# Kernel tuning notes

Hardware: AMD Instinct MI355X
Metric: run time of the kernel (lower is better)

Reference implementation:

```python
import jax, jax.numpy as jnp
import numpy as np


def setup_inputs() -> dict:
    key = jax.random.key(0)
    k1, k2, k3 = jax.random.split(key, 3)
    B, S, D = 2, 2048, 1024
    N_COMPRESS, RANK = 64, 64
    x = jax.random.normal(k1, (B, S, D), dtype=jnp.float32)
    router_w = jax.random.normal(k2, (N_COMPRESS, D), dtype=jnp.float32) * (1.0 / np.sqrt(D))
    # compress neurons (orthogonal-init in torch; gaussian scaled is fine for a numeric baseline)
    neurons = jax.random.normal(k3, (N_COMPRESS, D, RANK), dtype=jnp.float32) * (1.0 / np.sqrt(D))
    return {"x": x, "router_w": router_w, "neurons": neurons}


TOP_K = 2


def reference(x, router_w, neurons):
    # x: [B,S,D], router_w: [N,D], neurons: [N,D,R]
    B, S, D = x.shape
    R = neurons.shape[-1]
    scores = jnp.einsum('bsd,nd->bsn', x, router_w)            # [B,S,N]
    topk_scores, topk_idx = jax.lax.top_k(scores, TOP_K)       # [B,S,K]
    topk_weights = jax.nn.softmax(topk_scores, axis=-1)        # [B,S,K]
    output = jnp.zeros((B, S, R), dtype=x.dtype)
    for i in range(TOP_K):  # small fixed loop, mirrors original slot-wise combine
        idx = topk_idx[:, :, i]                                # [B,S]
        sel = neurons[idx]                                     # [B,S,D,R] gather
        proj = jnp.einsum('bsd,bsdr->bsr', x, sel)             # per-token matvec
        output = output + topk_weights[:, :, i:i + 1] * proj
    return output, topk_idx, topk_weights
```

## Files before the change

### kernel.cpp

```cpp
#include <hip/hip_runtime.h>
#include <hip/hip_bf16.h>


typedef unsigned short u16;
typedef unsigned int u32;
typedef __attribute__((ext_vector_type(8))) short short8;
typedef __attribute__((ext_vector_type(4))) float f32x4;

__device__ __forceinline__ float bf2f(u16 u) {
    u32 v = ((u32)u) << 16; float f; __builtin_memcpy(&f, &v, 4); return f;
}
__device__ __forceinline__ u16 f2bf(float f) {
    u32 u; __builtin_memcpy(&u, &f, 4);
    u32 r = u + 0x7fff + ((u >> 16) & 1);
    return (u16)(r >> 16);
}
__device__ __forceinline__ u32 pack2(float a, float b) {
    return ((u32)f2bf(b) << 16) | (u32)f2bf(a);
}

#define T_TOKENS 4096
#define DDIM 1024
#define NEXP 64
#define RDIM 64
#define LCAP 1024
#define OUT_IDX_OFF 262144
#define OUT_W_OFF 270336

struct LdBF {
    const u16* p;
    __device__ __forceinline__ float4 ld4(size_t i) const {
        ushort4 v = *(const ushort4*)(p + i);
        return make_float4(bf2f(v.x), bf2f(v.y), bf2f(v.z), bf2f(v.w));
    }
    __device__ __forceinline__ float ld1(size_t i) const { return bf2f(p[i]); }
};
struct LdF32 {
    const float* p;
    __device__ __forceinline__ float4 ld4(size_t i) const { return *(const float4*)(p + i); }
    __device__ __forceinline__ float ld1(size_t i) const { return p[i]; }
};

__device__ __forceinline__ int detect_f32(const u16* x, int* lds_cnt) {
    if (threadIdx.x == 0) *lds_cnt = 0;
    __syncthreads();
    if (threadIdx.x < 256) {
        unsigned e = (x[threadIdx.x] >> 7) & 0xFF;
        if (e >= 0x68 && e <= 0x88) atomicAdd(lds_cnt, 1);
    }
    __syncthreads();
    int f = (*lds_cnt < 200) ? 1 : 0;
    __syncthreads();
    return f;
}

template <class LD>
__device__ __forceinline__ void score_body(LD xld, LD rwld,
                                           float* xs , float* wt ,
                                           float* sc ,
                                           float* out, float* wsW,
                                           int* wsCnt, int* wsList) {
    const int tid = threadIdx.x;
    const size_t t0 = (size_t)blockIdx.x * 16;
    const int wv = tid >> 6;
    const int lane = tid & 63;
    const int tg = lane & 1;
    const int eg = (lane >> 1) & 7;
    const int kql = (lane >> 4) & 3;
    const int dd = 4 * kql + 16 * wv;

    {
        float4 z = make_float4(0.f, 0.f, 0.f, 0.f);
        ((float4*)out)[(size_t)blockIdx.x * 256 + tid] = z;
    }

    const int sm = tid >> 4;
    const int sd4 = (tid & 15) * 4;

    float acc[8][8];
#pragma unroll
    for (int mi = 0; mi < 8; ++mi)
#pragma unroll
        for (int ei = 0; ei < 8; ++ei) acc[mi][ei] = 0.f;

    {
        float4 px = xld.ld4((t0 + sm) * DDIM + sd4);
        *(float4*)&xs[sm * 68 + sd4] = px;
#pragma unroll
        for (int h = 0; h < 4; ++h) {
            int i4 = tid + h * 256;
            float4 pw = rwld.ld4((size_t)(i4 >> 4) * DDIM + (i4 & 15) * 4);
            *(float4*)&wt[(i4 >> 4) * 68 + (i4 & 15) * 4] = pw;
        }
    }
    __syncthreads();

    for (int kc = 0; kc < 16; ++kc) {
        float4 px; float4 pw[4];
        if (kc < 15) {
            px = xld.ld4((t0 + sm) * DDIM + (kc + 1) * 64 + sd4);
#pragma unroll
            for (int h = 0; h < 4; ++h) {
                int i4 = tid + h * 256;
                pw[h] = rwld.ld4((size_t)(i4 >> 4) * DDIM + (kc + 1) * 64 + (i4 & 15) * 4);
            }
        }

        const float* xsb = xs + (kc & 1) * (16 * 68);
        const float* wtb = wt + (kc & 1) * (64 * 68);
        float4 xv[8], wv4[8];
#pragma unroll
        for (int mi = 0; mi < 8; ++mi)
            xv[mi] = *(const float4*)&xsb[(tg + 2 * mi) * 68 + dd];
#pragma unroll
        for (int ei = 0; ei < 8; ++ei)
            wv4[ei] = *(const float4*)&wtb[(eg + 8 * ei) * 68 + dd];
#pragma unroll
        for (int mi = 0; mi < 8; ++mi)
#pragma unroll
            for (int ei = 0; ei < 8; ++ei)
                acc[mi][ei] += xv[mi].x * wv4[ei].x + xv[mi].y * wv4[ei].y +
                               xv[mi].z * wv4[ei].z + xv[mi].w * wv4[ei].w;

        if (kc < 15) {
            float* xsn = xs + ((kc + 1) & 1) * (16 * 68);
            float* wtn = wt + ((kc + 1) & 1) * (64 * 68);
            *(float4*)&xsn[sm * 68 + sd4] = px;
#pragma unroll
            for (int h = 0; h < 4; ++h) {
                int i4 = tid + h * 256;
                *(float4*)&wtn[(i4 >> 4) * 68 + (i4 & 15) * 4] = pw[h];
            }
            __syncthreads();
        }
    }

#pragma unroll
    for (int mi = 0; mi < 8; ++mi)
#pragma unroll
        for (int ei = 0; ei < 8; ++ei) {
            float v = acc[mi][ei];
            v += __shfl_xor(v, 16, 64);
            v += __shfl_xor(v, 32, 64);
            acc[mi][ei] = v;
        }
    __syncthreads();

    for (int w = 0; w < 4; ++w) {
        if (wv == w && kql == 0) {
#pragma unroll
            for (int mi = 0; mi < 8; ++mi)
#pragma unroll
                for (int ei = 0; ei < 8; ++ei) {
                    int idx = (tg + 2 * mi) * 65 + eg + 8 * ei;
                    sc[idx] = (w == 0) ? acc[mi][ei] : sc[idx] + acc[mi][ei];
                }
        }
        __syncthreads();
    }

    if (tid < 16) {
        const float* s = &sc[tid * 65];
        float best = -1e30f, secv = -1e30f;
        int bi = 0, si = 0;
        for (int j = 0; j < NEXP; ++j) {
            float v = s[j];
            if (v > best) { secv = best; si = bi; best = v; bi = j; }
            else if (v > secv) { secv = v; si = j; }
        }
        float w0 = 1.0f / (1.0f + expf(secv - best));
        float w1 = 1.0f - w0;
        size_t t = t0 + tid;
        out[OUT_IDX_OFF + t * 2 + 0] = (float)bi;
        out[OUT_IDX_OFF + t * 2 + 1] = (float)si;
        out[OUT_W_OFF + t * 2 + 0] = w0;
        out[OUT_W_OFF + t * 2 + 1] = w1;
        wsW[t * 2 + 0] = w0;
        wsW[t * 2 + 1] = w1;
        int p0 = atomicAdd(&wsCnt[bi], 1);
        if (p0 < LCAP) wsList[bi * LCAP + p0] = (int)(t * 2 + 0);
        int p1 = atomicAdd(&wsCnt[si], 1);
        if (p1 < LCAP) wsList[si * LCAP + p1] = (int)(t * 2 + 1);
    }
}

__global__ __launch_bounds__(256, 1) void score_topk(const void* x, const void* rw,
                                                     float* out, float* wsW,
                                                     int* wsCnt, int* wsList) {
    __shared__ float xs[2 * 16 * 68];
    __shared__ float wt[2 * 64 * 68];
    __shared__ float sc[16 * 65];
    __shared__ int dc;
    int f = detect_f32((const u16*)x, &dc);
    if (f)
        score_body(LdF32{(const float*)x}, LdF32{(const float*)rw}, xs, wt, sc, out, wsW, wsCnt, wsList);
    else
        score_body(LdBF{(const u16*)x}, LdBF{(const u16*)rw}, xs, wt, sc, out, wsW, wsCnt, wsList);
}

template <class LD>
__device__ __forceinline__ void egemm_body(LD xld, LD nld,
                                           const int* wsCnt, const int* wsList,
                                           const float* wsW, float* out,
                                           u16* Ab , u16* Bb ,
                                           int* entL ) {
    const int tid = threadIdx.x;
    const int e = blockIdx.x & 63;
    const int ti = blockIdx.x >> 6;
    const int cntE = min(wsCnt[e], LCAP);
    const int base = ti * 16;
    if (base >= cntE) return;
    const int valid = min(16, cntE - base);
    const int wv = tid >> 6;
    const int lane = tid & 63;
    const int l15 = lane & 15, quad = lane >> 4;
    const size_t nbase = (size_t)e * (DDIM * RDIM);

    if (tid < 16)
        entL[tid] = wsList[e * LCAP + base + min(tid, valid - 1)];
    __syncthreads();

    const int rowA = tid & 15;
    const int kq0 = tid >> 4;
    const size_t ttA = (size_t)(entL[rowA] >> 1) * DDIM;

    f32x4 acc = {0.f, 0.f, 0.f, 0.f};

    for (int kc = 0; kc < 8; ++kc) {
        const int k0c = kc * 128;
        if (kc > 0) __syncthreads();
#pragma unroll
        for (int h = 0; h < 4; ++h) {
            int u = tid + h * 256;
            int rq = u & 15, kp = u >> 4;
            float4 g0 = nld.ld4(nbase + (size_t)(k0c + 2 * kp) * RDIM + 4 * rq);
            float4 g1 = nld.ld4(nbase + (size_t)(k0c + 2 * kp + 1) * RDIM + 4 * rq);
            u32* bw = (u32*)Bb;
            bw[(4 * rq + 0) * 68 + kp] = pack2(g0.x, g1.x);
            bw[(4 * rq + 1) * 68 + kp] = pack2(g0.y, g1.y);
            bw[(4 * rq + 2) * 68 + kp] = pack2(g0.z, g1.z);
            bw[(4 * rq + 3) * 68 + kp] = pack2(g0.w, g1.w);
        }
        {
            float4 ga0 = xld.ld4(ttA + k0c + 4 * kq0);
            float4 ga1 = xld.ld4(ttA + k0c + 4 * (kq0 + 16));
            u32* aw = (u32*)Ab;
            aw[rowA * 68 + 2 * kq0 + 0]  = pack2(ga0.x, ga0.y);
            aw[rowA * 68 + 2 * kq0 + 1]  = pack2(ga0.z, ga0.w);
            aw[rowA * 68 + 2 * kq0 + 32] = pack2(ga1.x, ga1.y);
            aw[rowA * 68 + 2 * kq0 + 33] = pack2(ga1.z, ga1.w);
        }
        __syncthreads();

#pragma unroll
        for (int ko = 0; ko < 4; ++ko) {
            int kofs = ko * 32 + quad * 8;
            short8 bfr = *(const short8*)&Bb[(16 * wv + l15) * 136 + kofs];
            short8 af = *(const short8*)&Ab[l15 * 136 + kofs];
            acc = __builtin_amdgcn_mfma_f32_16x16x32_bf16(af, bfr, acc, 0, 0, 0);
        }
    }

#pragma unroll
    for (int reg = 0; reg < 4; ++reg) {
        int m = quad * 4 + reg;
        if (m < valid) {
            int t2 = entL[m];
            atomicAdd(&out[(size_t)(t2 >> 1) * RDIM + 16 * wv + l15], wsW[t2] * acc[reg]);
        }
    }
}

__global__ __launch_bounds__(256) void expert_gemm(const void* x, const void* neurons,
                                                   const int* wsCnt, const int* wsList,
                                                   const float* wsW, float* out) {
    __shared__ u16 Ab[16 * 136];
    __shared__ u16 Bb[64 * 136];
    __shared__ int entL[16];
    __shared__ int dc;
    int f = detect_f32((const u16*)x, &dc);
    if (f)
        egemm_body(LdF32{(const float*)x}, LdF32{(const float*)neurons}, wsCnt, wsList, wsW, out, Ab, Bb, entL);
    else
        egemm_body(LdBF{(const u16*)x}, LdBF{(const u16*)neurons}, wsCnt, wsList, wsW, out, Ab, Bb, entL);
}

extern "C" void kernel_launch(void* const* d_in, const int* in_sizes, int n_in,
                              void* d_out, int out_size, void* d_ws, size_t ws_size,
                              hipStream_t stream) {
    const void* x = d_in[0];
    const void* rw = d_in[1];
    const void* neurons = d_in[2];
    float* out = (float*)d_out;

    char* wsc = (char*)d_ws;
    float* wsW = (float*)wsc;
    int* wsCnt = (int*)(wsc + 32 * 1024);
    int* wsList = (int*)((char*)wsCnt + 256);

    hipMemsetAsync(wsCnt, 0, 256, stream);
    score_topk<<<256, 256, 0, stream>>>(x, rw, out, wsW, wsCnt, wsList);
    expert_gemm<<<1024, 256, 0, stream>>>(x, neurons, wsCnt, wsList, wsW, out);
}
```

Before: 151.3 us.

## Split router score GEMM over K into partial blocks plus combine kernel

Router scoring now splits the D=1024 reduction into four 256-wide chunks, so 1024 blocks write partial scores to workspace. A new combine kernel sums the partials, zeroes the output and does top-2, softmax and expert bucketing. This gives 4x more blocks than the previous 256-block launch, which left many CUs idle on a 256-CU part. The price is an extra kernel launch, a workspace round-trip for the partials, and losing double-buffered LDS inside the shorter K loop.

```diff
diff --git a/kernel.cpp b/kernel.cpp
--- a/kernel.cpp
+++ b/kernel.cpp
@@ -55,13 +55,14 @@
 }
 
 template <class LD>
-__device__ __forceinline__ void score_body(LD xld, LD rwld,
+__device__ __forceinline__ void spart_body(LD xld, LD rwld,
                                            float* xs , float* wt ,
-                                           float* sc ,
-                                           float* out, float* wsW,
-                                           int* wsCnt, int* wsList) {
+                                           float* sc , float* psc) {
     const int tid = threadIdx.x;
-    const size_t t0 = (size_t)blockIdx.x * 16;
+    const int g = blockIdx.x >> 2;
+    const int p = blockIdx.x & 3;
+    const size_t t0 = (size_t)g * 16;
+    const int kbase = p * 256;
     const int wv = tid >> 6;
     const int lane = tid & 63;
     const int tg = lane & 1;
@@ -69,11 +70,6 @@
     const int kql = (lane >> 4) & 3;
     const int dd = 4 * kql + 16 * wv;
 
-    {
-        float4 z = make_float4(0.f, 0.f, 0.f, 0.f);
-        ((float4*)out)[(size_t)blockIdx.x * 256 + tid] = z;
-    }
-
     const int sm = tid >> 4;
     const int sd4 = (tid & 15) * 4;
 
@@ -83,56 +79,46 @@
 #pragma unroll
         for (int ei = 0; ei < 8; ++ei) acc[mi][ei] = 0.f;
 
-    {
-        float4 px = xld.ld4((t0 + sm) * DDIM + sd4);
+    float4 px = xld.ld4((t0 + sm) * DDIM + kbase + sd4);
+    float4 pw[4];
+#pragma unroll
+    for (int h = 0; h < 4; ++h) {
+        int i4 = tid + h * 256;
+        pw[h] = rwld.ld4((size_t)(i4 >> 4) * DDIM + kbase + (i4 & 15) * 4);
+    }
+
+    for (int kc = 0; kc < 4; ++kc) {
+        if (kc > 0) __syncthreads();
         *(float4*)&xs[sm * 68 + sd4] = px;
 #pragma unroll
         for (int h = 0; h < 4; ++h) {
             int i4 = tid + h * 256;
-            float4 pw = rwld.ld4((size_t)(i4 >> 4) * DDIM + (i4 & 15) * 4);
-            *(float4*)&wt[(i4 >> 4) * 68 + (i4 & 15) * 4] = pw;
-        }
-    }
-    __syncthreads();
-
-    for (int kc = 0; kc < 16; ++kc) {
-        float4 px; float4 pw[4];
-        if (kc < 15) {
-            px = xld.ld4((t0 + sm) * DDIM + (kc + 1) * 64 + sd4);
+            *(float4*)&wt[(i4 >> 4) * 68 + (i4 & 15) * 4] = pw[h];
+        }
+        __syncthreads();
+
+        if (kc < 3) {
+            px = xld.ld4((t0 + sm) * DDIM + kbase + (kc + 1) * 64 + sd4);
 #pragma unroll
             for (int h = 0; h < 4; ++h) {
                 int i4 = tid + h * 256;
-                pw[h] = rwld.ld4((size_t)(i4 >> 4) * DDIM + (kc + 1) * 64 + (i4 & 15) * 4);
+                pw[h] = rwld.ld4((size_t)(i4 >> 4) * DDIM + kbase + (kc + 1) * 64 + (i4 & 15) * 4);
             }
         }
 
-        const float* xsb = xs + (kc & 1) * (16 * 68);
-        const float* wtb = wt + (kc & 1) * (64 * 68);
         float4 xv[8], wv4[8];
 #pragma unroll
         for (int mi = 0; mi < 8; ++mi)
-            xv[mi] = *(const float4*)&xsb[(tg + 2 * mi) * 68 + dd];
+            xv[mi] = *(const float4*)&xs[(tg + 2 * mi) * 68 + dd];
 #pragma unroll
         for (int ei = 0; ei < 8; ++ei)
-            wv4[ei] = *(const float4*)&wtb[(eg + 8 * ei) * 68 + dd];
+            wv4[ei] = *(const float4*)&wt[(eg + 8 * ei) * 68 + dd];
 #pragma unroll
         for (int mi = 0; mi < 8; ++mi)
 #pragma unroll
             for (int ei = 0; ei < 8; ++ei)
                 acc[mi][ei] += xv[mi].x * wv4[ei].x + xv[mi].y * wv4[ei].y +
                                xv[mi].z * wv4[ei].z + xv[mi].w * wv4[ei].w;
-
-        if (kc < 15) {
-            float* xsn = xs + ((kc + 1) & 1) * (16 * 68);
-            float* wtn = wt + ((kc + 1) & 1) * (64 * 68);
-            *(float4*)&xsn[sm * 68 + sd4] = px;
-#pragma unroll
-            for (int h = 0; h < 4; ++h) {
-                int i4 = tid + h * 256;
-                *(float4*)&wtn[(i4 >> 4) * 68 + (i4 & 15) * 4] = pw[h];
-            }
-            __syncthreads();
-        }
     }
 
 #pragma unroll
@@ -158,6 +144,53 @@
         }
         __syncthreads();
     }
+
+    {
+        int m = tid >> 4, e4 = (tid & 15) * 4;
+        float4 v = *(const float4*)&sc[m * 65 + e4];
+        *(float4*)&psc[((t0 + m) * 4 + p) * 64 + e4] = v;
+    }
+}
+
+__global__ __launch_bounds__(256) void score_partial(const void* x, const void* rw,
+                                                     float* psc) {
+    __shared__ float xs[16 * 68];
+    __shared__ float wt[64 * 68];
+    __shared__ float sc[16 * 65];
+    __shared__ int dc;
+    int f = detect_f32((const u16*)x, &dc);
+    if (f)
+        spart_body(LdF32{(const float*)x}, LdF32{(const float*)rw}, xs, wt, sc, psc);
+    else
+        spart_body(LdBF{(const u16*)x}, LdBF{(const u16*)rw}, xs, wt, sc, psc);
+}
+
+__global__ __launch_bounds__(256) void combine_topk(const float* __restrict__ psc,
+                                                    float* out, float* wsW,
+                                                    int* wsCnt, int* wsList) {
+    __shared__ float sc[16 * 65];
+    const int tid = threadIdx.x;
+    const size_t t0 = (size_t)blockIdx.x * 16;
+
+    {
+        float4 z = make_float4(0.f, 0.f, 0.f, 0.f);
+        ((float4*)out)[(size_t)blockIdx.x * 256 + tid] = z;
+    }
+
+    {
+        int m = tid >> 4, e4 = (tid & 15) * 4;
+        const float* pp = &psc[(t0 + m) * 4 * 64 + e4];
+        float4 s = *(const float4*)(pp + 0 * 64);
+        float4 s1 = *(const float4*)(pp + 1 * 64);
+        float4 s2 = *(const float4*)(pp + 2 * 64);
+        float4 s3 = *(const float4*)(pp + 3 * 64);
+        s.x = ((s.x + s1.x) + s2.x) + s3.x;
+        s.y = ((s.y + s1.y) + s2.y) + s3.y;
+        s.z = ((s.z + s1.z) + s2.z) + s3.z;
+        s.w = ((s.w + s1.w) + s2.w) + s3.w;
+        *(float4*)&sc[m * 65 + e4] = s;
+    }
+    __syncthreads();
 
     if (tid < 16) {
         const float* s = &sc[tid * 65];
@@ -182,20 +215,6 @@
         int p1 = atomicAdd(&wsCnt[si], 1);
         if (p1 < LCAP) wsList[si * LCAP + p1] = (int)(t * 2 + 1);
     }
-}
-
-__global__ __launch_bounds__(256, 1) void score_topk(const void* x, const void* rw,
-                                                     float* out, float* wsW,
-                                                     int* wsCnt, int* wsList) {
-    __shared__ float xs[2 * 16 * 68];
-    __shared__ float wt[2 * 64 * 68];
-    __shared__ float sc[16 * 65];
-    __shared__ int dc;
-    int f = detect_f32((const u16*)x, &dc);
-    if (f)
-        score_body(LdF32{(const float*)x}, LdF32{(const float*)rw}, xs, wt, sc, out, wsW, wsCnt, wsList);
-    else
-        score_body(LdBF{(const u16*)x}, LdBF{(const u16*)rw}, xs, wt, sc, out, wsW, wsCnt, wsList);
 }
 
 template <class LD>
@@ -297,8 +316,10 @@
     float* wsW = (float*)wsc;
     int* wsCnt = (int*)(wsc + 32 * 1024);
     int* wsList = (int*)((char*)wsCnt + 256);
+    float* psc = (float*)((char*)wsList + (size_t)NEXP * LCAP * 4);
 
     hipMemsetAsync(wsCnt, 0, 256, stream);
-    score_topk<<<256, 256, 0, stream>>>(x, rw, out, wsW, wsCnt, wsList);
+    score_partial<<<1024, 256, 0, stream>>>(x, rw, psc);
+    combine_topk<<<256, 256, 0, stream>>>(psc, out, wsW, wsCnt, wsList);
     expert_gemm<<<1024, 256, 0, stream>>>(x, neurons, wsCnt, wsList, wsW, out);
 }
```

Result: faster. 138.4 us (-8.5%).
